# Performance work log

Measured on AMD Instinct MI355X. Metric: run time of the kernel, lower is better.

Reference implementation:

```python
import jax, jax.numpy as jnp
import numpy as np
from jax import lax

PAD, HOP, SCALES = 2, 256, (4, 8, 8)
AUX_D = 32  # res_out_dims // 4
BN_EPS = 1e-5


def _bn(x, g, b):
    # eval-mode BatchNorm1d with running_mean=0, running_var=1; x: [B,C,L]
    inv = g / jnp.sqrt(1.0 + BN_EPS)
    return x * inv[:, None] + b[:, None]


def _mel_resnet(m, conv_in_w, bn0_g, bn0_b, res_c1, res_c2,
                res_bn1_g, res_bn1_b, res_bn2_g, res_bn2_b,
                conv_out_w, conv_out_b):
    # m: [B, feat, frames]; conv_in kernel 5, VALID
    x = lax.conv_general_dilated(m, conv_in_w, (1,), 'VALID',
                                 dimension_numbers=('NCH', 'OIH', 'NCH'))
    x = jax.nn.relu(_bn(x, bn0_g, bn0_b))
    n_blocks = res_c1.shape[0]
    for i in range(n_blocks):  # kernel-1 convs are channel matmuls
        r = x
        h = jnp.einsum('bcl,oc->bol', x, res_c1[i])
        h = jax.nn.relu(_bn(h, res_bn1_g[i], res_bn1_b[i]))
        h = jnp.einsum('bcl,oc->bol', h, res_c2[i])
        x = _bn(h, res_bn2_g[i], res_bn2_b[i]) + r
    x = jnp.einsum('bcl,oc->bol', x, conv_out_w) + conv_out_b[None, :, None]
    return x  # [B, res_out_dims, frames-4]


def _upsample(mels, up_ws):
    # mels: [B, feat, frames] -> [B, T, feat]
    m = mels[:, None]  # [B,1,feat,frames]
    for s, w in zip(SCALES, up_ws):
        m = jnp.repeat(m, s, axis=-1)  # Stretch2d along width
        m = lax.conv_general_dilated(m, w, (1, 1), [(0, 0), (s, s)],
                                     dimension_numbers=('NCHW', 'OIHW', 'NCHW'))
    indent = PAD * HOP
    m = m[:, 0, :, indent:-indent]  # [B, feat, T]
    return jnp.transpose(m, (0, 2, 1))


def _gru(x, wih, whh, bih, bhh):
    # PyTorch GRU semantics, batch_first, h0 = 0. x: [B,T,D]
    B = x.shape[0]
    H = whh.shape[1]
    xp = (x @ wih.T + bih).transpose(1, 0, 2)  # [T,B,3H], input proj hoisted

    def step(h, xt):
        gh = h @ whh.T + bhh
        xr, xz, xn = jnp.split(xt, 3, axis=-1)
        hr, hz, hn = jnp.split(gh, 3, axis=-1)
        r = jax.nn.sigmoid(xr + hr)
        z = jax.nn.sigmoid(xz + hz)
        n = jnp.tanh(xn + r * hn)
        h_new = (1.0 - z) * n + z * h
        return h_new, h_new

    h0 = jnp.zeros((B, H), x.dtype)
    _, ys = lax.scan(step, h0, xp)
    return ys.transpose(1, 0, 2)  # [B,T,H]


def wavernn_forward(x, mels, conv_in_w, bn0_g, bn0_b, res_c1, res_c2,
                    res_bn1_g, res_bn1_b, res_bn2_g, res_bn2_b,
                    conv_out_w, conv_out_b, up_w0, up_w1, up_w2,
                    I_w, I_b, r1_wih, r1_whh, r1_bih, r1_bhh,
                    r2_wih, r2_whh, r2_bih, r2_bhh,
                    fc1_w, fc1_b, fc2_w, fc2_b, fc3_w, fc3_b):
    total_scale = int(np.prod(SCALES))
    aux = _mel_resnet(mels, conv_in_w, bn0_g, bn0_b, res_c1, res_c2,
                      res_bn1_g, res_bn1_b, res_bn2_g, res_bn2_b,
                      conv_out_w, conv_out_b)
    aux = jnp.repeat(aux, total_scale, axis=-1)      # resnet_stretch
    aux = jnp.transpose(aux, (0, 2, 1))              # [B,T,res_out]
    m_up = _upsample(mels, (up_w0, up_w1, up_w2))    # [B,T,feat]

    a1 = aux[:, :, 0 * AUX_D:1 * AUX_D]
    a2 = aux[:, :, 1 * AUX_D:2 * AUX_D]
    a3 = aux[:, :, 2 * AUX_D:3 * AUX_D]
    a4 = aux[:, :, 3 * AUX_D:4 * AUX_D]

    h = jnp.concatenate([x[..., None], m_up, a1], axis=2) @ I_w.T + I_b
    h = _gru(h, r1_wih, r1_whh, r1_bih, r1_bhh) + h
    h = _gru(jnp.concatenate([h, a2], axis=2), r2_wih, r2_whh, r2_bih, r2_bhh) + h
    h = jax.nn.relu(jnp.concatenate([h, a3], axis=2) @ fc1_w.T + fc1_b)
    h = jax.nn.relu(jnp.concatenate([h, a4], axis=2) @ fc2_w.T + fc2_b)
    return h @ fc3_w.T + fc3_b  # [B,T,n_classes]


def setup_inputs() -> dict:
    key = jax.random.key(0)
    ks = jax.random.split(key, 24)
    B, FRAMES, FEAT = 4, 54, 80
    C, H, FC, NC = 128, 512, 512, 1024
    T = (FRAMES - 2 * PAD) * HOP  # 12800
    s = 0.05
    rn = lambda k, shp, sc=s: jax.random.normal(k, shp, dtype=jnp.float32) * sc
    d = {}
    d['x'] = jax.random.normal(ks[0], (B, T), dtype=jnp.float32)
    d['mels'] = jax.random.normal(ks[1], (B, FEAT, FRAMES), dtype=jnp.float32)
    d['conv_in_w'] = rn(ks[2], (C, FEAT, 5))
    d['bn0_g'] = jnp.ones((C,), jnp.float32)
    d['bn0_b'] = jnp.zeros((C,), jnp.float32)
    d['res_c1'] = rn(ks[3], (10, C, C))
    d['res_c2'] = rn(ks[4], (10, C, C))
    d['res_bn1_g'] = jnp.ones((10, C), jnp.float32)
    d['res_bn1_b'] = jnp.zeros((10, C), jnp.float32)
    d['res_bn2_g'] = jnp.ones((10, C), jnp.float32)
    d['res_bn2_b'] = jnp.zeros((10, C), jnp.float32)
    d['conv_out_w'] = rn(ks[5], (C, C))
    d['conv_out_b'] = jnp.zeros((C,), jnp.float32)
    d['up_w0'] = jnp.full((1, 1, 1, 9), 1.0 / 9.0, jnp.float32)
    d['up_w1'] = jnp.full((1, 1, 1, 17), 1.0 / 17.0, jnp.float32)
    d['up_w2'] = jnp.full((1, 1, 1, 17), 1.0 / 17.0, jnp.float32)
    d['I_w'] = rn(ks[6], (H, FEAT + AUX_D + 1))
    d['I_b'] = jnp.zeros((H,), jnp.float32)
    d['r1_wih'] = rn(ks[7], (3 * H, H))
    d['r1_whh'] = rn(ks[8], (3 * H, H))
    d['r1_bih'] = jnp.zeros((3 * H,), jnp.float32)
    d['r1_bhh'] = jnp.zeros((3 * H,), jnp.float32)
    d['r2_wih'] = rn(ks[9], (3 * H, H + AUX_D))
    d['r2_whh'] = rn(ks[10], (3 * H, H))
    d['r2_bih'] = jnp.zeros((3 * H,), jnp.float32)
    d['r2_bhh'] = jnp.zeros((3 * H,), jnp.float32)
    d['fc1_w'] = rn(ks[11], (FC, H + AUX_D))
    d['fc1_b'] = jnp.zeros((FC,), jnp.float32)
    d['fc2_w'] = rn(ks[12], (FC, FC + AUX_D))
    d['fc2_b'] = jnp.zeros((FC,), jnp.float32)
    d['fc3_w'] = rn(ks[13], (NC, FC))
    d['fc3_b'] = jnp.zeros((NC,), jnp.float32)
    return d


def reference(x, mels, conv_in_w, bn0_g, bn0_b, res_c1, res_c2,
              res_bn1_g, res_bn1_b, res_bn2_g, res_bn2_b,
              conv_out_w, conv_out_b, up_w0, up_w1, up_w2,
              I_w, I_b, r1_wih, r1_whh, r1_bih, r1_bhh,
              r2_wih, r2_whh, r2_bih, r2_bhh,
              fc1_w, fc1_b, fc2_w, fc2_b, fc3_w, fc3_b):
    return wavernn_forward(x, mels, conv_in_w, bn0_g, bn0_b, res_c1, res_c2,
                           res_bn1_g, res_bn1_b, res_bn2_g, res_bn2_b,
                           conv_out_w, conv_out_b, up_w0, up_w1, up_w2,
                           I_w, I_b, r1_wih, r1_whh, r1_bih, r1_bhh,
                           r2_wih, r2_whh, r2_bih, r2_bhh,
                           fc1_w, fc1_b, fc2_w, fc2_b, fc3_w, fc3_b)
```

## Files before the change

### kernel.cpp

```cpp
#include <hip/hip_runtime.h>

#define T_LEN  12800
#define BATCH  4
#define HID    512
#define NFEAT  80
#define FRAMES 54
#define CCH    128
#define LRES   50
#define M_ROWS (BATCH * T_LEN)

#define SCOPE_SYS __HIP_MEMORY_SCOPE_SYSTEM

__global__ __launch_bounds__(128)
void k_conv_in(const float* __restrict__ mels, const float* __restrict__ w,
               const float* __restrict__ g, const float* __restrict__ bb,
               float* __restrict__ out) {
    int blk = blockIdx.x;
    int b = blk / LRES, l = blk % LRES;
    int o = threadIdx.x;
    __shared__ float ms[NFEAT * 5];
    for (int i = o; i < NFEAT * 5; i += 128) {
        int c = i / 5, k = i % 5;
        ms[i] = mels[(b * NFEAT + c) * FRAMES + l + k];
    }
    __syncthreads();
    const float* wr = w + o * NFEAT * 5;
    float s = 0.f;
    for (int i = 0; i < NFEAT * 5; ++i) s = fmaf(ms[i], wr[i], s);
    float inv = g[o] * rsqrtf(1.f + 1e-5f);
    s = s * inv + bb[o];
    out[(b * CCH + o) * LRES + l] = fmaxf(s, 0.f);
}

template <int MODE>
__global__ __launch_bounds__(128)
void k_ein(const float* __restrict__ x, const float* __restrict__ w,
           const float* __restrict__ g, const float* __restrict__ bb,
           const float* __restrict__ res, float* __restrict__ out) {
    int blk = blockIdx.x;
    int b = blk / LRES, l = blk % LRES;
    int o = threadIdx.x;
    __shared__ float xs[CCH];
    xs[o] = x[(b * CCH + o) * LRES + l];
    __syncthreads();
    const float* wr = w + o * CCH;
    float s = 0.f;
#pragma unroll 8
    for (int c = 0; c < CCH; ++c) s = fmaf(xs[c], wr[c], s);
    float v;
    if (MODE == 2) {
        v = s + bb[o];
    } else {
        float inv = g[o] * rsqrtf(1.f + 1e-5f);
        v = s * inv + bb[o];
        if (MODE == 0) v = fmaxf(v, 0.f);
        else           v = v + res[(b * CCH + o) * LRES + l];
    }
    out[(b * CCH + o) * LRES + l] = v;
}

__global__ __launch_bounds__(256)
void k_auxrep(const float* __restrict__ aux_s, float* __restrict__ aux_t) {
    int idx = blockIdx.x * 256 + threadIdx.x;
    int ch = idx & 127;
    int bt = idx >> 7;
    int t = bt % T_LEN, b = bt / T_LEN;
    aux_t[idx] = aux_s[(b * CCH + ch) * LRES + (t >> 8)];
}

__global__ __launch_bounds__(256)
void k_up1(const float* __restrict__ mels, const float* __restrict__ w0, float* __restrict__ s1) {
    int idx = blockIdx.x * 256 + threadIdx.x;
    int i = idx % 216; int bc = idx / 216;
    float s = 0.f;
#pragma unroll
    for (int k = 0; k < 9; ++k) {
        int q = i + k - 4;
        if (q >= 0 && q < 216) s = fmaf(w0[k], mels[bc * FRAMES + (q >> 2)], s);
    }
    s1[idx] = s;
}
__global__ __launch_bounds__(256)
void k_up2(const float* __restrict__ s1, const float* __restrict__ w1, float* __restrict__ s2) {
    int idx = blockIdx.x * 256 + threadIdx.x;
    int j = idx % 1728; int bc = idx / 1728;
    float s = 0.f;
#pragma unroll
    for (int k = 0; k < 17; ++k) {
        int q = j + k - 8;
        if (q >= 0 && q < 1728) s = fmaf(w1[k], s1[bc * 216 + (q >> 3)], s);
    }
    s2[idx] = s;
}
__global__ __launch_bounds__(256)
void k_up3(const float* __restrict__ s2, const float* __restrict__ w2, float* __restrict__ mup) {
    int idx = blockIdx.x * 256 + threadIdx.x;
    int c = idx % NFEAT; int bt = idx / NFEAT;
    int t = bt % T_LEN; int b = bt / T_LEN;
    const float* src = s2 + (b * NFEAT + c) * 1728;
    float s = 0.f;
#pragma unroll
    for (int k = 0; k < 17; ++k) s = fmaf(w2[k], src[(t + 504 + k) >> 3], s);
    mup[idx] = s;
}

template <int ACT>
__global__ __launch_bounds__(256)
void gemm_f32(const float* __restrict__ A1, int lda1, int K1,
              const float* __restrict__ A2, int lda2, int K2,
              const float* __restrict__ A3, int lda3, int K3,
              const float* __restrict__ W, const float* __restrict__ bias,
              float* __restrict__ C, int N, int K) {
    __shared__ float As[8][128];
    __shared__ float Bs[8][128];
    int tid = threadIdx.x;
    int n0 = blockIdx.x * 128, m0 = blockIdx.y * 128;
    int tx = tid & 15, ty = tid >> 4;
    int row = tid >> 1;
    int kc = (tid & 1) * 4;
    float acc[8][8];
#pragma unroll
    for (int r = 0; r < 8; ++r)
#pragma unroll
        for (int c = 0; c < 8; ++c) acc[r][c] = 0.f;

    for (int k0 = 0; k0 < K; k0 += 8) {
#pragma unroll
        for (int e = 0; e < 4; ++e) {
            int gk = k0 + kc + e;
            int m = m0 + row;
            float v = 0.f;
            if (gk < K1)            v = A1[(size_t)m * lda1 + gk];
            else if (gk < K1 + K2)  v = A2[(size_t)m * lda2 + (gk - K1)];
            else if (gk < K)        v = A3[(size_t)m * lda3 + (gk - K1 - K2)];
            As[kc + e][row] = v;
            float wv = (gk < K) ? W[(size_t)(n0 + row) * K + gk] : 0.f;
            Bs[kc + e][row] = wv;
        }
        __syncthreads();
#pragma unroll
        for (int kk = 0; kk < 8; ++kk) {
            float a[8], bv[8];
#pragma unroll
            for (int h = 0; h < 2; ++h) {
                float4 t4 = *(const float4*)&As[kk][ty * 8 + h * 4];
                a[h * 4 + 0] = t4.x; a[h * 4 + 1] = t4.y; a[h * 4 + 2] = t4.z; a[h * 4 + 3] = t4.w;
                float4 u4 = *(const float4*)&Bs[kk][tx * 8 + h * 4];
                bv[h * 4 + 0] = u4.x; bv[h * 4 + 1] = u4.y; bv[h * 4 + 2] = u4.z; bv[h * 4 + 3] = u4.w;
            }
#pragma unroll
            for (int r = 0; r < 8; ++r)
#pragma unroll
                for (int c = 0; c < 8; ++c) acc[r][c] = fmaf(a[r], bv[c], acc[r][c]);
        }
        __syncthreads();
    }
#pragma unroll
    for (int r = 0; r < 8; ++r) {
        int m = m0 + ty * 8 + r;
        float* co = C + (size_t)m * N + n0 + tx * 8;
#pragma unroll
        for (int c = 0; c < 8; ++c) {
            float v = acc[r][c] + bias[n0 + tx * 8 + c];
            if (ACT) v = fmaxf(v, 0.f);
            co[c] = v;
        }
    }
}

__global__ __launch_bounds__(384)
void k_gru(const float* __restrict__ xp, const float* __restrict__ whh,
           const float* __restrict__ bhh, const float* __restrict__ skip,
           float* __restrict__ hseq, float* hbuf, int* flags) {
    int blk = blockIdx.x;
    int cb = blk & 7;
    if (cb >= BATCH) return;
    int wg = blk >> 3;
    int tid = threadIdx.x;
    int ch0 = wg * 32;
    int rg = tid >> 4;
    int p = tid & 15;

    float* hb = hbuf + cb * 2 * HID;
    int* flg = flags + cb * 16;

    float w[128];
#pragma unroll
    for (int j = 0; j < 4; ++j) {
        int lr = rg * 4 + j;
        int R = (lr >> 5) * HID + ch0 + (lr & 31);
        const float* src = whh + (size_t)R * HID + p * 32;
#pragma unroll
        for (int q = 0; q < 8; ++q) {
            float4 v = *(const float4*)&src[q * 4];
            w[j * 32 + q * 4 + 0] = v.x; w[j * 32 + q * 4 + 1] = v.y;
            w[j * 32 + q * 4 + 2] = v.z; w[j * 32 + q * 4 + 3] = v.w;
        }
    }
    float bR = 0.f, bZ = 0.f, bN = 0.f;
    if (tid < 32) {
        bR = bhh[ch0 + tid];
        bZ = bhh[HID + ch0 + tid];
        bN = bhh[2 * HID + ch0 + tid];
    }

    __shared__ float h_lds[16 * 36];
    __shared__ float gh_lds[96];
    const size_t brow = (size_t)cb * T_LEN;
    int spin_budget = 1 << 22;

    for (int t = 0; t < T_LEN; ++t) {
        float xr = 0.f, xz = 0.f, xn = 0.f, skv = 0.f;
        if (tid < 32) {
            const float* xpt = xp + (brow + t) * 1536;
            xr = xpt[ch0 + tid];
            xz = xpt[HID + ch0 + tid];
            xn = xpt[2 * HID + ch0 + tid];
            skv = skip[(brow + t) * HID + ch0 + tid];
        }

        if (t == 0) {
            h_lds[tid] = 0.f;
            if (tid < 192) h_lds[384 + tid] = 0.f;
        } else if (tid < 64) {
            while (true) {
                int v = (tid < 16)
                    ? __hip_atomic_load(&flg[tid], __ATOMIC_RELAXED, SCOPE_SYS)
                    : t;
                if (__all(v >= t)) break;
                if (--spin_budget < 0) break;
            }
            __builtin_amdgcn_sched_barrier(0);
            const float* hc = hb + (t & 1) * HID;
            float hv[8];
#pragma unroll
            for (int j = 0; j < 8; ++j)
                hv[j] = __hip_atomic_load(&hc[tid + 64 * j], __ATOMIC_RELAXED, SCOPE_SYS);
#pragma unroll
            for (int j = 0; j < 8; ++j) {
                int i = tid + 64 * j;
                h_lds[(i >> 5) * 36 + (i & 31)] = hv[j];
            }
        }
        __syncthreads();

        float a0 = 0.f, a1 = 0.f, a2 = 0.f, a3 = 0.f;
#pragma unroll
        for (int q = 0; q < 8; ++q) {
            float4 hv4 = *(const float4*)&h_lds[p * 36 + q * 4];
            float hh[4] = {hv4.x, hv4.y, hv4.z, hv4.w};
#pragma unroll
            for (int e = 0; e < 4; ++e) {
                int i = q * 4 + e;
                a0 = fmaf(w[i],      hh[e], a0);
                a1 = fmaf(w[32 + i], hh[e], a1);
                a2 = fmaf(w[64 + i], hh[e], a2);
                a3 = fmaf(w[96 + i], hh[e], a3);
            }
        }
        a0 += __shfl_xor(a0, 1); a0 += __shfl_xor(a0, 2); a0 += __shfl_xor(a0, 4); a0 += __shfl_xor(a0, 8);
        a1 += __shfl_xor(a1, 1); a1 += __shfl_xor(a1, 2); a1 += __shfl_xor(a1, 4); a1 += __shfl_xor(a1, 8);
        a2 += __shfl_xor(a2, 1); a2 += __shfl_xor(a2, 2); a2 += __shfl_xor(a2, 4); a2 += __shfl_xor(a2, 8);
        a3 += __shfl_xor(a3, 1); a3 += __shfl_xor(a3, 2); a3 += __shfl_xor(a3, 4); a3 += __shfl_xor(a3, 8);
        if (p == 0) {
            gh_lds[rg * 4 + 0] = a0;
            gh_lds[rg * 4 + 1] = a1;
            gh_lds[rg * 4 + 2] = a2;
            gh_lds[rg * 4 + 3] = a3;
        }
        __syncthreads();

        if (tid < 64) {
            if (tid < 32) {
                float hr = gh_lds[tid], hz = gh_lds[32 + tid], hn = gh_lds[64 + tid];
                float rr = __fdividef(1.f, 1.f + __expf(-(xr + hr + bR)));
                float zz = __fdividef(1.f, 1.f + __expf(-(xz + hz + bZ)));
                float ax = xn + rr * (hn + bN);
                float e2 = __expf(2.f * ax);
                float nn = 1.f - __fdividef(2.f, e2 + 1.f);
                float hprev = h_lds[wg * 36 + tid];
                float hnew = (1.f - zz) * nn + zz * hprev;
                float* hnx = hb + ((t + 1) & 1) * HID;
                __hip_atomic_store(&hnx[ch0 + tid], hnew, __ATOMIC_RELAXED, SCOPE_SYS);
                hseq[(brow + t) * HID + ch0 + tid] = hnew + skv;
            }
            asm volatile("s_waitcnt vmcnt(0)" ::: "memory");
            if (tid == 0)
                __hip_atomic_store(&flg[wg], t + 1, __ATOMIC_RELAXED, SCOPE_SYS);
        }
    }
}

extern "C" void kernel_launch(void* const* d_in, const int* in_sizes, int n_in,
                              void* d_out, int out_size, void* d_ws, size_t ws_size,
                              hipStream_t stream) {
    (void)in_sizes; (void)n_in; (void)out_size; (void)ws_size;
    const float* x         = (const float*)d_in[0];
    const float* mels      = (const float*)d_in[1];
    const float* conv_in_w = (const float*)d_in[2];
    const float* bn0_g     = (const float*)d_in[3];
    const float* bn0_b     = (const float*)d_in[4];
    const float* res_c1    = (const float*)d_in[5];
    const float* res_c2    = (const float*)d_in[6];
    const float* res_bn1_g = (const float*)d_in[7];
    const float* res_bn1_b = (const float*)d_in[8];
    const float* res_bn2_g = (const float*)d_in[9];
    const float* res_bn2_b = (const float*)d_in[10];
    const float* conv_out_w= (const float*)d_in[11];
    const float* conv_out_b= (const float*)d_in[12];
    const float* up_w0     = (const float*)d_in[13];
    const float* up_w1     = (const float*)d_in[14];
    const float* up_w2     = (const float*)d_in[15];
    const float* I_w       = (const float*)d_in[16];
    const float* I_b       = (const float*)d_in[17];
    const float* r1_wih    = (const float*)d_in[18];
    const float* r1_whh    = (const float*)d_in[19];
    const float* r1_bih    = (const float*)d_in[20];
    const float* r1_bhh    = (const float*)d_in[21];
    const float* r2_wih    = (const float*)d_in[22];
    const float* r2_whh    = (const float*)d_in[23];
    const float* r2_bih    = (const float*)d_in[24];
    const float* r2_bhh    = (const float*)d_in[25];
    const float* fc1_w     = (const float*)d_in[26];
    const float* fc1_b     = (const float*)d_in[27];
    const float* fc2_w     = (const float*)d_in[28];
    const float* fc2_b     = (const float*)d_in[29];
    const float* fc3_w     = (const float*)d_in[30];
    const float* fc3_b     = (const float*)d_in[31];

    char* ws = (char*)d_ws;
    size_t off = 0;
    auto alloc = [&](size_t bytes) {
        char* p = ws + off;
        off += (bytes + 255) & ~(size_t)255;
        return p;
    };
    int*   flags1 = (int*)  alloc(256);
    int*   flags2 = (int*)  alloc(256);
    float* hbuf1  = (float*)alloc(4 * 2 * HID * 4);
    float* hbuf2  = (float*)alloc(4 * 2 * HID * 4);
    float* rnA    = (float*)alloc((size_t)BATCH * CCH * LRES * 4);
    float* rnB    = (float*)alloc((size_t)BATCH * CCH * LRES * 4);
    float* aux_s  = (float*)alloc((size_t)BATCH * CCH * LRES * 4);
    float* s1     = (float*)alloc((size_t)BATCH * NFEAT * 216 * 4);
    float* s2     = (float*)alloc((size_t)BATCH * NFEAT * 1728 * 4);
    float* mup    = (float*)alloc((size_t)BATCH * T_LEN * NFEAT * 4);
    float* auxt   = (float*)alloc((size_t)BATCH * T_LEN * CCH * 4);
    float* h0     = (float*)alloc((size_t)M_ROWS * HID * 4);
    float* xp     = (float*)alloc((size_t)M_ROWS * 1536 * 4);
    float* h1     = (float*)alloc((size_t)M_ROWS * HID * 4);
    float* h2     = (float*)alloc((size_t)M_ROWS * HID * 4);
    float* f1 = h0;
    float* f2 = h1;

    hipMemsetAsync(flags1, 0, 512, stream);

    k_conv_in<<<BATCH * LRES, 128, 0, stream>>>(mels, conv_in_w, bn0_g, bn0_b, rnA);
    for (int i = 0; i < 10; ++i) {
        k_ein<0><<<BATCH * LRES, 128, 0, stream>>>(rnA, res_c1 + (size_t)i * CCH * CCH,
            res_bn1_g + i * CCH, res_bn1_b + i * CCH, nullptr, rnB);
        k_ein<1><<<BATCH * LRES, 128, 0, stream>>>(rnB, res_c2 + (size_t)i * CCH * CCH,
            res_bn2_g + i * CCH, res_bn2_b + i * CCH, rnA, rnA);
    }
    k_ein<2><<<BATCH * LRES, 128, 0, stream>>>(rnA, conv_out_w, nullptr, conv_out_b, nullptr, aux_s);
    k_auxrep<<<(BATCH * T_LEN * CCH) / 256, 256, 0, stream>>>(aux_s, auxt);

    k_up1<<<(BATCH * NFEAT * 216) / 256, 256, 0, stream>>>(mels, up_w0, s1);
    k_up2<<<(BATCH * NFEAT * 1728) / 256, 256, 0, stream>>>(s1, up_w1, s2);
    k_up3<<<(BATCH * T_LEN * NFEAT) / 256, 256, 0, stream>>>(s2, up_w2, mup);

    gemm_f32<0><<<dim3(512 / 128, M_ROWS / 128), 256, 0, stream>>>(
        x, 1, 1, mup, NFEAT, NFEAT, auxt, CCH, 32, I_w, I_b, h0, 512, 113);
    gemm_f32<0><<<dim3(1536 / 128, M_ROWS / 128), 256, 0, stream>>>(
        h0, HID, HID, nullptr, 0, 0, nullptr, 0, 0, r1_wih, r1_bih, xp, 1536, 512);
    k_gru<<<128, 384, 0, stream>>>(xp, r1_whh, r1_bhh, h0, h1, hbuf1, flags1);
    gemm_f32<0><<<dim3(1536 / 128, M_ROWS / 128), 256, 0, stream>>>(
        h1, HID, HID, auxt + 32, CCH, 32, nullptr, 0, 0, r2_wih, r2_bih, xp, 1536, 544);
    k_gru<<<128, 384, 0, stream>>>(xp, r2_whh, r2_bhh, h1, h2, hbuf2, flags2);
    gemm_f32<1><<<dim3(512 / 128, M_ROWS / 128), 256, 0, stream>>>(
        h2, HID, HID, auxt + 64, CCH, 32, nullptr, 0, 0, fc1_w, fc1_b, f1, 512, 544);
    gemm_f32<1><<<dim3(512 / 128, M_ROWS / 128), 256, 0, stream>>>(
        f1, HID, HID, auxt + 96, CCH, 32, nullptr, 0, 0, fc2_w, fc2_b, f2, 512, 544);
    gemm_f32<0><<<dim3(1024 / 128, M_ROWS / 128), 256, 0, stream>>>(
        f2, HID, HID, nullptr, 0, 0, nullptr, 0, 0, fc3_w, fc3_b, (float*)d_out, 1024, 512);
}
```

Measured before the change: 64.55 ms.

## Pipeline both GRU layers and the layer-2 input projection in one persistent kernel

Merges the two sequential GRU recurrences and the GRU-2 input-projection GEMM into one persistent kernel. Layer 1 runs in some workgroups while worker workgroups compute the layer-2 input projection chunk by chunk into a 64-step ring buffer, and the layer-2 GRU consumes it concurrently through flag-based wavefront synchronisation. This is meant to overlap the two serial recurrences instead of running them back to back. It relies on all 152 blocks being co-resident and on system-scope spin-waits, so there is a deadlock risk if residency fails, and ring back-pressure can stall the pipeline.

```diff
diff --git a/kernel.cpp b/kernel.cpp
--- a/kernel.cpp
+++ b/kernel.cpp
@@ -8,6 +8,8 @@
 #define CCH    128
 #define LRES   50
 #define M_ROWS (BATCH * T_LEN)
+#define RING   64
+#define NWRK   24
 
 #define SCOPE_SYS __HIP_MEMORY_SCOPE_SYSTEM
 
@@ -168,21 +170,20 @@
     }
 }
 
-__global__ __launch_bounds__(384)
-void k_gru(const float* __restrict__ xp, const float* __restrict__ whh,
-           const float* __restrict__ bhh, const float* __restrict__ skip,
-           float* __restrict__ hseq, float* hbuf, int* flags) {
-    int blk = blockIdx.x;
-    int cb = blk & 7;
-    if (cb >= BATCH) return;
-    int wg = blk >> 3;
+template <int MODE>
+__device__ __forceinline__ void gru_cluster(
+    int cb, int wg,
+    const float* __restrict__ xp, const float* __restrict__ whh,
+    const float* __restrict__ bhh, const float* __restrict__ skip,
+    float* __restrict__ hseq, float* hb, int* flg, const int* prog,
+    float* smem)
+{
     int tid = threadIdx.x;
     int ch0 = wg * 32;
     int rg = tid >> 4;
     int p = tid & 15;
-
-    float* hb = hbuf + cb * 2 * HID;
-    int* flg = flags + cb * 16;
+    float* h_lds = smem;
+    float* gh_lds = smem + 576;
 
     float w[128];
 #pragma unroll
@@ -204,33 +205,52 @@
         bN = bhh[2 * HID + ch0 + tid];
     }
 
-    __shared__ float h_lds[16 * 36];
-    __shared__ float gh_lds[96];
     const size_t brow = (size_t)cb * T_LEN;
     int spin_budget = 1 << 22;
 
     for (int t = 0; t < T_LEN; ++t) {
         float xr = 0.f, xz = 0.f, xn = 0.f, skv = 0.f;
-        if (tid < 32) {
+        if (MODE == 1 && tid < 32) {
             const float* xpt = xp + (brow + t) * 1536;
             xr = xpt[ch0 + tid];
             xz = xpt[HID + ch0 + tid];
             xn = xpt[2 * HID + ch0 + tid];
             skv = skip[(brow + t) * HID + ch0 + tid];
         }
+        if (MODE == 2 && tid < 64) {
+            while (true) {
+                int v;
+                if (tid < 16)      v = __hip_atomic_load(&flg[tid], __ATOMIC_RELAXED, SCOPE_SYS);
+                else if (tid < 16 + NWRK)
+                                   v = __hip_atomic_load(&prog[tid - 16], __ATOMIC_RELAXED, SCOPE_SYS) - 1;
+                else               v = t;
+                if (__all(v >= t)) break;
+                if (--spin_budget < 0) break;
+            }
+            __builtin_amdgcn_sched_barrier(0);
+            if (tid < 32) {
+                const float* xpt = xp + ((size_t)(t & (RING - 1)) * BATCH + cb) * 1536;
+                xr = __hip_atomic_load(&xpt[ch0 + tid], __ATOMIC_RELAXED, SCOPE_SYS);
+                xz = __hip_atomic_load(&xpt[HID + ch0 + tid], __ATOMIC_RELAXED, SCOPE_SYS);
+                xn = __hip_atomic_load(&xpt[2 * HID + ch0 + tid], __ATOMIC_RELAXED, SCOPE_SYS);
+                skv = __hip_atomic_load(&skip[(brow + t) * HID + ch0 + tid], __ATOMIC_RELAXED, SCOPE_SYS);
+            }
+        }
 
         if (t == 0) {
             h_lds[tid] = 0.f;
             if (tid < 192) h_lds[384 + tid] = 0.f;
         } else if (tid < 64) {
-            while (true) {
-                int v = (tid < 16)
-                    ? __hip_atomic_load(&flg[tid], __ATOMIC_RELAXED, SCOPE_SYS)
-                    : t;
-                if (__all(v >= t)) break;
-                if (--spin_budget < 0) break;
-            }
-            __builtin_amdgcn_sched_barrier(0);
+            if (MODE == 1) {
+                while (true) {
+                    int v = (tid < 16)
+                        ? __hip_atomic_load(&flg[tid], __ATOMIC_RELAXED, SCOPE_SYS)
+                        : t;
+                    if (__all(v >= t)) break;
+                    if (--spin_budget < 0) break;
+                }
+                __builtin_amdgcn_sched_barrier(0);
+            }
             const float* hc = hb + (t & 1) * HID;
             float hv[8];
 #pragma unroll
@@ -282,12 +302,154 @@
                 float hnew = (1.f - zz) * nn + zz * hprev;
                 float* hnx = hb + ((t + 1) & 1) * HID;
                 __hip_atomic_store(&hnx[ch0 + tid], hnew, __ATOMIC_RELAXED, SCOPE_SYS);
-                hseq[(brow + t) * HID + ch0 + tid] = hnew + skv;
+                float ov = hnew + skv;
+                if (MODE == 1)
+                    __hip_atomic_store(&hseq[(brow + t) * HID + ch0 + tid], ov, __ATOMIC_RELAXED, SCOPE_SYS);
+                else
+                    hseq[(brow + t) * HID + ch0 + tid] = ov;
             }
             asm volatile("s_waitcnt vmcnt(0)" ::: "memory");
             if (tid == 0)
                 __hip_atomic_store(&flg[wg], t + 1, __ATOMIC_RELAXED, SCOPE_SYS);
         }
+    }
+}
+
+__global__ __launch_bounds__(384, 2)
+void k_mega(const float* __restrict__ xp1, const float* __restrict__ whh1,
+            const float* __restrict__ bhh1, const float* __restrict__ h0,
+            float* __restrict__ hseq1,
+            const float* __restrict__ r2_wih, const float* __restrict__ r2_bih,
+            const float* __restrict__ auxt, float* __restrict__ xp2r,
+            const float* __restrict__ whh2, const float* __restrict__ bhh2,
+            float* __restrict__ hseq2,
+            float* hbuf, int* flags)
+{
+    __shared__ float smem[4 * 552];
+    int blk = blockIdx.x;
+    if (blk < 128) {
+        int x8 = blk & 7;
+        int wg = blk >> 3;
+        if (x8 < 4)
+            gru_cluster<1>(x8, wg, xp1, whh1, bhh1, h0, hseq1,
+                           hbuf + x8 * 2 * HID, flags + x8 * 16, nullptr, smem);
+        else
+            gru_cluster<2>(x8 - 4, wg, xp2r, whh2, bhh2, hseq1, hseq2,
+                           hbuf + (4 + (x8 - 4)) * 2 * HID,
+                           flags + 64 + (x8 - 4) * 16, flags + 128, smem);
+        return;
+    }
+
+    int wid = blk - 128;
+    int tid = threadIdx.x;
+    bool act = tid < 256;
+    int ocg = (tid & 255) >> 3;
+    int seg = tid & 7;
+    int obase = wid * 64;
+    float (*hx)[552] = (float(*)[552])smem;
+
+    float w2[2][68];
+    float bz[2] = {0.f, 0.f};
+    if (act) {
+#pragma unroll
+        for (int j = 0; j < 2; ++j) {
+            int o = obase + j * 32 + ocg;
+            const float* src = r2_wih + (size_t)o * 544 + seg * 68;
+#pragma unroll
+            for (int q = 0; q < 17; ++q) {
+                float4 v = *(const float4*)&src[q * 4];
+                w2[j][q * 4 + 0] = v.x; w2[j][q * 4 + 1] = v.y;
+                w2[j][q * 4 + 2] = v.z; w2[j][q * 4 + 3] = v.w;
+            }
+            bz[j] = r2_bih[o];
+        }
+    }
+    int* flg1 = flags;
+    int* flg2 = flags + 64;
+    int* prog = flags + 128;
+    int spin_budget = 1 << 22;
+
+    for (int c0 = 0; c0 < T_LEN; c0 += 8) {
+        if (tid < 64) {
+            int need1 = c0 + 8;
+            int need2 = c0 - (RING - 8);
+            while (true) {
+                int v1 = __hip_atomic_load(&flg1[tid], __ATOMIC_RELAXED, SCOPE_SYS);
+                int v2 = (need2 > 0)
+                    ? __hip_atomic_load(&flg2[tid], __ATOMIC_RELAXED, SCOPE_SYS)
+                    : need2;
+                if (__all(v1 >= need1 && v2 >= need2)) break;
+                if (--spin_budget < 0) break;
+            }
+            __builtin_amdgcn_sched_barrier(0);
+        }
+        __syncthreads();
+        for (int t = c0; t < c0 + 8; ++t) {
+            if (act) {
+#pragma unroll
+                for (int k = 0; k < 8; ++k) {
+                    int j = tid + 256 * k;
+                    int b = j >> 9, i = j & 511;
+                    hx[b][i] = __hip_atomic_load(
+                        &hseq1[((size_t)b * T_LEN + t) * HID + i],
+                        __ATOMIC_RELAXED, SCOPE_SYS);
+                }
+                if (tid < 128) {
+                    int b = tid >> 5, i = tid & 31;
+                    hx[b][512 + i] = auxt[((size_t)b * T_LEN + t) * CCH + 32 + i];
+                }
+            }
+            __syncthreads();
+            if (act) {
+                float acc[2][4] = {{0.f,0.f,0.f,0.f},{0.f,0.f,0.f,0.f}};
+                int s68 = seg * 68;
+#pragma unroll
+                for (int q = 0; q < 17; ++q) {
+                    float4 h0v = *(const float4*)&hx[0][s68 + q * 4];
+                    float4 h1v = *(const float4*)&hx[1][s68 + q * 4];
+                    float4 h2v = *(const float4*)&hx[2][s68 + q * 4];
+                    float4 h3v = *(const float4*)&hx[3][s68 + q * 4];
+                    float hb0[4] = {h0v.x, h0v.y, h0v.z, h0v.w};
+                    float hb1[4] = {h1v.x, h1v.y, h1v.z, h1v.w};
+                    float hb2[4] = {h2v.x, h2v.y, h2v.z, h2v.w};
+                    float hb3[4] = {h3v.x, h3v.y, h3v.z, h3v.w};
+#pragma unroll
+                    for (int u = 0; u < 4; ++u) {
+                        float w0 = w2[0][q * 4 + u], w1 = w2[1][q * 4 + u];
+                        acc[0][0] = fmaf(w0, hb0[u], acc[0][0]);
+                        acc[0][1] = fmaf(w0, hb1[u], acc[0][1]);
+                        acc[0][2] = fmaf(w0, hb2[u], acc[0][2]);
+                        acc[0][3] = fmaf(w0, hb3[u], acc[0][3]);
+                        acc[1][0] = fmaf(w1, hb0[u], acc[1][0]);
+                        acc[1][1] = fmaf(w1, hb1[u], acc[1][1]);
+                        acc[1][2] = fmaf(w1, hb2[u], acc[1][2]);
+                        acc[1][3] = fmaf(w1, hb3[u], acc[1][3]);
+                    }
+                }
+#pragma unroll
+                for (int j = 0; j < 2; ++j)
+#pragma unroll
+                    for (int b = 0; b < 4; ++b) {
+                        float a = acc[j][b];
+                        a += __shfl_xor(a, 1); a += __shfl_xor(a, 2); a += __shfl_xor(a, 4);
+                        acc[j][b] = a;
+                    }
+                if (seg == 0) {
+#pragma unroll
+                    for (int j = 0; j < 2; ++j)
+#pragma unroll
+                        for (int b = 0; b < 4; ++b)
+                            __hip_atomic_store(
+                                &xp2r[((size_t)(t & (RING - 1)) * BATCH + b) * 1536
+                                      + obase + j * 32 + ocg],
+                                acc[j][b] + bz[j], __ATOMIC_RELAXED, SCOPE_SYS);
+                }
+            }
+            __syncthreads();
+        }
+        asm volatile("s_waitcnt vmcnt(0)" ::: "memory");
+        if (tid == 0)
+            __hip_atomic_store(&prog[wid], c0 + 8, __ATOMIC_RELAXED, SCOPE_SYS);
     }
 }
 
@@ -335,10 +497,9 @@
         off += (bytes + 255) & ~(size_t)255;
         return p;
     };
-    int*   flags1 = (int*)  alloc(256);
-    int*   flags2 = (int*)  alloc(256);
-    float* hbuf1  = (float*)alloc(4 * 2 * HID * 4);
-    float* hbuf2  = (float*)alloc(4 * 2 * HID * 4);
+    int*   flagsA = (int*)  alloc(1024);
+    float* hbuf   = (float*)alloc(8 * 2 * HID * 4);
+    float* xp2r   = (float*)alloc((size_t)RING * BATCH * 1536 * 4);
     float* rnA    = (float*)alloc((size_t)BATCH * CCH * LRES * 4);
     float* rnB    = (float*)alloc((size_t)BATCH * CCH * LRES * 4);
     float* aux_s  = (float*)alloc((size_t)BATCH * CCH * LRES * 4);
@@ -353,7 +514,7 @@
     float* f1 = h0;
     float* f2 = h1;
 
-    hipMemsetAsync(flags1, 0, 512, stream);
+    hipMemsetAsync(flagsA, 0, 1024, stream);
 
     k_conv_in<<<BATCH * LRES, 128, 0, stream>>>(mels, conv_in_w, bn0_g, bn0_b, rnA);
     for (int i = 0; i < 10; ++i) {
@@ -373,10 +534,11 @@
         x, 1, 1, mup, NFEAT, NFEAT, auxt, CCH, 32, I_w, I_b, h0, 512, 113);
     gemm_f32<0><<<dim3(1536 / 128, M_ROWS / 128), 256, 0, stream>>>(
         h0, HID, HID, nullptr, 0, 0, nullptr, 0, 0, r1_wih, r1_bih, xp, 1536, 512);
-    k_gru<<<128, 384, 0, stream>>>(xp, r1_whh, r1_bhh, h0, h1, hbuf1, flags1);
-    gemm_f32<0><<<dim3(1536 / 128, M_ROWS / 128), 256, 0, stream>>>(
-        h1, HID, HID, auxt + 32, CCH, 32, nullptr, 0, 0, r2_wih, r2_bih, xp, 1536, 544);
-    k_gru<<<128, 384, 0, stream>>>(xp, r2_whh, r2_bhh, h1, h2, hbuf2, flags2);
+
+    k_mega<<<152, 384, 0, stream>>>(xp, r1_whh, r1_bhh, h0, h1,
+                                    r2_wih, r2_bih, auxt, xp2r,
+                                    r2_whh, r2_bhh, h2, hbuf, flagsA);
+
     gemm_f32<1><<<dim3(512 / 128, M_ROWS / 128), 256, 0, stream>>>(
         h2, HID, HID, auxt + 64, CCH, 32, nullptr, 0, 0, fc1_w, fc1_b, f1, 512, 544);
     gemm_f32<1><<<dim3(512 / 128, M_ROWS / 128), 256, 0, stream>>>(
```

Measured after the change: 58.06 ms. 10.1% less time.
